# Optimization experiments

Hardware: AMD Instinct MI355X
Metric: run time of the kernel (lower is better)

Reference implementation:

```python
import jax, jax.numpy as jnp
import numpy as np

N_PATHS = 100000
N_STEPS = 512          # number of Euler steps; paths have N_STEPS+1 time points
DT = 0.004             # step_size (~1/250, daily)
KAPPA = 1.0
THETA = 0.04
SIGMA = 0.2
RHO = -0.7
S0 = 100.0
V0 = 0.04


def setup_inputs() -> dict:
    key = jax.random.key(0)
    z = jax.random.normal(key, (N_PATHS, N_STEPS, 2), dtype=jnp.float32)
    return {"z": z}


def reference(z):
    # Euler-Maruyama simulation of the Heston SDE with full-truncation clamp:
    #   dS = S * sqrt(v) dW1
    #   dv = kappa*(theta - v) dt + sigma*sqrt(v) dW2,  corr(dW1,dW2)=rho
    sqdt = jnp.sqrt(jnp.float32(DT))
    c = jnp.sqrt(jnp.float32(1.0 - RHO * RHO))

    def step(carry, zt):
        s, v = carry                      # each [N]
        vp = jnp.maximum(v, 0.0)
        sv = jnp.sqrt(vp)
        dW1 = sqdt * zt[:, 0]
        dW2 = RHO * dW1 + c * sqdt * zt[:, 1]
        s_new = s + s * sv * dW1
        v_new = jnp.maximum(v + KAPPA * (THETA - vp) * DT + SIGMA * sv * dW2, 0.0)
        return (s_new, v_new), (s_new, v_new)

    s0 = jnp.full((N_PATHS,), S0, dtype=z.dtype)
    v0 = jnp.full((N_PATHS,), V0, dtype=z.dtype)
    _, (ss, vs) = jax.lax.scan(step, (s0, v0), jnp.transpose(z, (1, 0, 2)))

    prices = jnp.concatenate([s0[None], ss], axis=0).T      # [N, T+1]
    variances = jnp.concatenate([v0[None], vs], axis=0).T   # [N, T+1]

    # variance-swap price: cumsum of variance * dt + analytic remaining leg L
    tau = jnp.linspace(N_STEPS * DT, 0.0, N_STEPS + 1).astype(z.dtype)  # [T+1]
    L = (variances - THETA) / KAPPA * (1.0 - jnp.exp(-KAPPA * tau)) + THETA * tau
    varswap = jnp.cumsum(variances, axis=1) * DT + L        # [N, T+1]

    # [N, T+1, 3] = (price, variance, varswap price)
    return jnp.stack([prices, variances, varswap], axis=-1)
```

## Files before the change

### kernel.cpp

```cpp
#include <hip/hip_runtime.h>


#define N_PATHS 100000
#define N_STEPS 512
#define TROW    1539
#define PB      64
#define SUB     16
#define NSUBTOT 32
#define NPH     8
#define PHSTEP  64
#define OSTR    195
#define ZSTR    34
#define DTc     0.004f
#define EDT     1.0040080107f

typedef float f32x4 __attribute__((ext_vector_type(4)));

__global__ __launch_bounds__(PB)
void heston_kernel(const float* __restrict__ z, float* __restrict__ out) {
    __shared__ float zl [PB * ZSTR];
    __shared__ float olB[PB * OSTR];

    const int tid = threadIdx.x;
    const int p0  = blockIdx.x * PB;
    const int lim = N_PATHS - p0;
    const bool full = (lim >= PB);

    const float sqdt = 0.06324555320f;
    const float csdt = 0.04516636050f;
    const float TAU0 = 2.048f;
    const float E0   = expf(-TAU0);

    int voff[8];
    #pragma unroll
    for (int j = 0; j < 8; ++j) {
        int pj = p0 + (tid >> 3) + 8 * j;
        if (pj > N_PATHS - 1) pj = N_PATHS - 1;
        voff[j] = pj * 4096 + (tid & 7) * 16;
    }
    const char* zb = (const char*)z;

    f32x4 fA[8], fB[8];
    #pragma unroll
    for (int j = 0; j < 8; ++j) fA[j] = *(const f32x4*)(zb + voff[j]);
    #pragma unroll
    for (int j = 0; j < 8; ++j) fB[j] = *(const f32x4*)(zb + voff[j] + 128);

    {
        const float vs0 = 0.08208f;
        #pragma unroll
        for (int k = 0; k < 3; ++k) {
            int idx = k * PB + tid;
            int pl = idx / 3, si = idx - pl * 3;
            if (pl < lim)
                out[(size_t)(p0 + pl) * TROW + si] = (si == 0) ? 100.0f : (si == 1) ? 0.04f : vs0;
        }
    }

    #pragma unroll
    for (int j = 0; j < 8; ++j) {
        float2* d = (float2*)&zl[((tid >> 3) + 8 * j) * ZSTR + (tid & 7) * 4];
        d[0] = make_float2(fA[j].x, fA[j].y);
        d[1] = make_float2(fA[j].z, fA[j].w);
    }

    float s = 100.0f, v = 0.04f, acc = 0.04f, tau = TAU0, e = E0;

    auto doSub = [&](int sc, int su, f32x4 (&fn)[8], f32x4 (&fw)[8]) {
        if (sc + 2 < NSUBTOT) {
            const int cn = (sc + 2) * 128;
            #pragma unroll
            for (int j = 0; j < 8; ++j) fn[j] = *(const f32x4*)(zb + voff[j] + cn);
        }
        const int dbase = su * (3 * SUB);
        #pragma unroll
        for (int dt = 0; dt < SUB; ++dt) {
            const float2 zz = *(const float2*)&zl[tid * ZSTR + 2 * dt];
            const float vp  = fmaxf(v, 0.0f);
            const float sv  = __builtin_amdgcn_sqrtf(vp);
            const float dW1 = sqdt * zz.x;
            const float dW2 = fmaf(-0.7f, dW1, csdt * zz.y);
            s = fmaf(s * sv, dW1, s);
            v = fmaxf(fmaf(0.2f * sv, dW2, fmaf(0.04f - vp, DTc, v)), 0.0f);
            acc += v;
            tau -= DTc;
            e *= EDT;
            const float vs = fmaf(acc, DTc, fmaf(0.04f, tau, (v - 0.04f) * (1.0f - e)));
            olB[tid * OSTR + dbase + 3 * dt    ] = s;
            olB[tid * OSTR + dbase + 3 * dt + 1] = v;
            olB[tid * OSTR + dbase + 3 * dt + 2] = vs;
        }
        #pragma unroll
        for (int j = 0; j < 8; ++j) {
            float2* d = (float2*)&zl[((tid >> 3) + 8 * j) * ZSTR + (tid & 7) * 4];
            d[0] = make_float2(fw[j].x, fw[j].y);
            d[1] = make_float2(fw[j].z, fw[j].w);
        }
    };

    for (int ph = 0; ph < NPH; ++ph) {
        const int sc0 = ph * 4;
        doSub(sc0    , 0, fA, fB);
        doSub(sc0 + 1, 1, fB, fA);
        doSub(sc0 + 2, 2, fA, fB);
        doSub(sc0 + 3, 3, fB, fA);

        float* gp = out + (size_t)p0 * TROW + 3 + (size_t)ph * (3 * PHSTEP);
        if (full) {
            #pragma unroll
            for (int pl = 0; pl < PB; ++pl) {
                gp[tid      ] = olB[pl * OSTR + tid      ];
                gp[tid +  64] = olB[pl * OSTR + tid +  64];
                gp[tid + 128] = olB[pl * OSTR + tid + 128];
                gp += TROW;
            }
        } else {
            #pragma unroll
            for (int pl = 0; pl < PB; ++pl) {
                if (pl < lim) {
                    gp[tid      ] = olB[pl * OSTR + tid      ];
                    gp[tid +  64] = olB[pl * OSTR + tid +  64];
                    gp[tid + 128] = olB[pl * OSTR + tid + 128];
                }
                gp += TROW;
            }
        }
    }
}

extern "C" void kernel_launch(void* const* d_in, const int* in_sizes, int n_in,
                              void* d_out, int out_size, void* d_ws, size_t ws_size,
                              hipStream_t stream) {
    const float* z = (const float*)d_in[0];
    float* out = (float*)d_out;
    const int nblocks = (N_PATHS + PB - 1) / PB;
    heston_kernel<<<nblocks, PB, 0, stream>>>(z, out);
}
```

Baseline: 341.2 us.

## Stage outputs as packed fp16 in LDS and load z per-thread directly

Removes the LDS transpose buffer for z so each thread loads its own path's normals straight into registers with one-chunk prefetch. Intermediate outputs are packed into fp16 pairs in shared memory, halving LDS footprint and allowing 128-step phases and fewer global write phases. The cost is that outputs are rounded to half precision before being written as fp32, which loses accuracy for values like prices near 100. Per-thread row loads are also poorly coalesced across lanes.

```diff
diff --git a/kernel.cpp b/kernel.cpp
--- a/kernel.cpp
+++ b/kernel.cpp
@@ -1,4 +1,5 @@
 #include <hip/hip_runtime.h>
+#include <hip/hip_fp16.h>
 
 
 #define N_PATHS 100000
@@ -6,123 +7,121 @@
 #define TROW    1539
 #define PB      64
 #define SUB     16
-#define NSUBTOT 32
-#define NPH     8
-#define PHSTEP  64
-#define OSTR    195
-#define ZSTR    34
+#define NSUB    32
+#define NPH     4
+#define PHSUB   8
+#define OSTR    193
 #define DTc     0.004f
 #define EDT     1.0040080107f
 
-typedef float f32x4 __attribute__((ext_vector_type(4)));
+typedef float  f32x4  __attribute__((ext_vector_type(4)));
+typedef __fp16 fp16x2 __attribute__((ext_vector_type(2)));
+
+__device__ __forceinline__ unsigned pk2(float a, float b) {
+    union { fp16x2 h; unsigned u; } cv;
+    cv.h = __builtin_amdgcn_cvt_pkrtz(a, b);
+    return cv.u;
+}
 
 __global__ __launch_bounds__(PB)
 void heston_kernel(const float* __restrict__ z, float* __restrict__ out) {
-    __shared__ float zl [PB * ZSTR];
-    __shared__ float olB[PB * OSTR];
+    __shared__ unsigned olB[PB * OSTR];
 
     const int tid = threadIdx.x;
     const int p0  = blockIdx.x * PB;
     const int lim = N_PATHS - p0;
-    const bool full = (lim >= PB);
+    const int p   = p0 + tid;
+    const int pc  = (p < N_PATHS) ? p : (N_PATHS - 1);
 
-    const float sqdt = 0.06324555320f;
-    const float csdt = 0.04516636050f;
-    const float TAU0 = 2.048f;
-    const float E0   = expf(-TAU0);
-
-    int voff[8];
-    #pragma unroll
-    for (int j = 0; j < 8; ++j) {
-        int pj = p0 + (tid >> 3) + 8 * j;
-        if (pj > N_PATHS - 1) pj = N_PATHS - 1;
-        voff[j] = pj * 4096 + (tid & 7) * 16;
-    }
-    const char* zb = (const char*)z;
+    const char* zp = (const char*)z + (size_t)pc * 4096;
 
     f32x4 fA[8], fB[8];
     #pragma unroll
-    for (int j = 0; j < 8; ++j) fA[j] = *(const f32x4*)(zb + voff[j]);
-    #pragma unroll
-    for (int j = 0; j < 8; ++j) fB[j] = *(const f32x4*)(zb + voff[j] + 128);
+    for (int j = 0; j < 8; ++j) fA[j] = *(const f32x4*)(zp + 16 * j);
 
     {
-        const float vs0 = 0.08208f;
         #pragma unroll
         for (int k = 0; k < 3; ++k) {
             int idx = k * PB + tid;
             int pl = idx / 3, si = idx - pl * 3;
             if (pl < lim)
-                out[(size_t)(p0 + pl) * TROW + si] = (si == 0) ? 100.0f : (si == 1) ? 0.04f : vs0;
+                out[(size_t)(p0 + pl) * TROW + si] =
+                    (si == 0) ? 100.0f : (si == 1) ? 0.04f : 0.08208f;
         }
     }
 
-    #pragma unroll
-    for (int j = 0; j < 8; ++j) {
-        float2* d = (float2*)&zl[((tid >> 3) + 8 * j) * ZSTR + (tid & 7) * 4];
-        d[0] = make_float2(fA[j].x, fA[j].y);
-        d[1] = make_float2(fA[j].z, fA[j].w);
-    }
+    float s = 100.0f, v = 0.04f, acc = 0.04f, tau = 2.048f, e = expf(-2.048f);
+    float sP = 0.f, vP = 0.f, vsP = 0.f;
 
-    float s = 100.0f, v = 0.04f, acc = 0.04f, tau = TAU0, e = E0;
-
-    auto doSub = [&](int sc, int su, f32x4 (&fn)[8], f32x4 (&fw)[8]) {
-        if (sc + 2 < NSUBTOT) {
-            const int cn = (sc + 2) * 128;
+    auto doSub = [&](int sc, int su, f32x4 (&cur)[8], f32x4 (&nxt)[8]) {
+        if (sc + 1 < NSUB) {
+            const char* zc = zp + (size_t)(sc + 1) * 128;
             #pragma unroll
-            for (int j = 0; j < 8; ++j) fn[j] = *(const f32x4*)(zb + voff[j] + cn);
+            for (int j = 0; j < 8; ++j) nxt[j] = *(const f32x4*)(zc + 16 * j);
         }
-        const int dbase = su * (3 * SUB);
+        const int dbase = tid * OSTR + su * 24;
         #pragma unroll
         for (int dt = 0; dt < SUB; ++dt) {
-            const float2 zz = *(const float2*)&zl[tid * ZSTR + 2 * dt];
+            const f32x4 q  = cur[dt >> 1];
+            const float z0 = (dt & 1) ? q.z : q.x;
+            const float z1 = (dt & 1) ? q.w : q.y;
+
             const float vp  = fmaxf(v, 0.0f);
             const float sv  = __builtin_amdgcn_sqrtf(vp);
-            const float dW1 = sqdt * zz.x;
-            const float dW2 = fmaf(-0.7f, dW1, csdt * zz.y);
+            const float dW1 = 0.06324555320f * z0;
+            const float dW2 = fmaf(-0.7f, dW1, 0.04516636050f * z1);
             s = fmaf(s * sv, dW1, s);
             v = fmaxf(fmaf(0.2f * sv, dW2, fmaf(0.04f - vp, DTc, v)), 0.0f);
             acc += v;
             tau -= DTc;
             e *= EDT;
             const float vs = fmaf(acc, DTc, fmaf(0.04f, tau, (v - 0.04f) * (1.0f - e)));
-            olB[tid * OSTR + dbase + 3 * dt    ] = s;
-            olB[tid * OSTR + dbase + 3 * dt + 1] = v;
-            olB[tid * OSTR + dbase + 3 * dt + 2] = vs;
-        }
-        #pragma unroll
-        for (int j = 0; j < 8; ++j) {
-            float2* d = (float2*)&zl[((tid >> 3) + 8 * j) * ZSTR + (tid & 7) * 4];
-            d[0] = make_float2(fw[j].x, fw[j].y);
-            d[1] = make_float2(fw[j].z, fw[j].w);
+
+            if (dt & 1) {
+                const int d = dbase + 3 * (dt >> 1);
+                olB[d + 0] = pk2(sP, vP);
+                olB[d + 1] = pk2(vsP, s);
+                olB[d + 2] = pk2(v, vs);
+            } else { sP = s; vP = v; vsP = vs; }
         }
     };
 
+    const int h  = tid & 1;
+    const int tq = tid >> 1;
+
     for (int ph = 0; ph < NPH; ++ph) {
-        const int sc0 = ph * 4;
-        doSub(sc0    , 0, fA, fB);
+        const int sc0 = ph * PHSUB;
+        doSub(sc0 + 0, 0, fA, fB);
         doSub(sc0 + 1, 1, fB, fA);
         doSub(sc0 + 2, 2, fA, fB);
         doSub(sc0 + 3, 3, fB, fA);
+        doSub(sc0 + 4, 4, fA, fB);
+        doSub(sc0 + 5, 5, fB, fA);
+        doSub(sc0 + 6, 6, fA, fB);
+        doSub(sc0 + 7, 7, fB, fA);
 
-        float* gp = out + (size_t)p0 * TROW + 3 + (size_t)ph * (3 * PHSTEP);
-        if (full) {
-            #pragma unroll
+        float* gp = out + (size_t)p0 * TROW + 3 + ph * 384;
+        if (lim >= PB) {
             for (int pl = 0; pl < PB; ++pl) {
-                gp[tid      ] = olB[pl * OSTR + tid      ];
-                gp[tid +  64] = olB[pl * OSTR + tid +  64];
-                gp[tid + 128] = olB[pl * OSTR + tid + 128];
-                gp += TROW;
+                const unsigned* lw = &olB[pl * OSTR + tq];
+                float* gr = gp + (size_t)pl * TROW + tid;
+                #pragma unroll
+                for (int k = 0; k < 6; ++k) {
+                    const unsigned w  = lw[32 * k];
+                    const unsigned us = h ? (w >> 16) : (w & 0xFFFFu);
+                    gr[64 * k] = __half2float(__ushort_as_half((unsigned short)us));
+                }
             }
         } else {
-            #pragma unroll
-            for (int pl = 0; pl < PB; ++pl) {
-                if (pl < lim) {
-                    gp[tid      ] = olB[pl * OSTR + tid      ];
-                    gp[tid +  64] = olB[pl * OSTR + tid +  64];
-                    gp[tid + 128] = olB[pl * OSTR + tid + 128];
+            for (int pl = 0; pl < lim; ++pl) {
+                const unsigned* lw = &olB[pl * OSTR + tq];
+                float* gr = gp + (size_t)pl * TROW + tid;
+                #pragma unroll
+                for (int k = 0; k < 6; ++k) {
+                    const unsigned w  = lw[32 * k];
+                    const unsigned us = h ? (w >> 16) : (w & 0xFFFFu);
+                    gr[64 * k] = __half2float(__ushort_as_half((unsigned short)us));
                 }
-                gp += TROW;
             }
         }
     }
```

Result: faster. 309.8 us (-9.2%).
